# Optimization experiments

Measured on AMD Instinct MI355X. Metric: run time of the kernel, lower is better.

Reference implementation:

```python
import jax, jax.numpy as jnp
import numpy as np

N_EMB = 512
EMB_DIM = 64
COMMITMENT_COST = 0.25


def setup_inputs() -> dict:
    key = jax.random.key(0)
    k1, k2 = jax.random.split(key)
    x = jax.random.normal(k1, (32, 64, 64, EMB_DIM), dtype=jnp.float32)
    init_bound = 1.0 / N_EMB
    embedding = jax.random.uniform(k2, (N_EMB, EMB_DIM), dtype=jnp.float32,
                                   minval=-init_bound, maxval=init_bound)
    return {"x": x, "embedding": embedding}


def reference(x, embedding):
    M, D = embedding.shape
    x_flat = jax.lax.stop_gradient(x).reshape(-1, D)  # [N, D]
    # distances = (-cdist(x, E))**2 == squared euclidean distance; argmin identical
    # to argmin over cdist, computed without forming sqrt:
    d2 = (jnp.sum(x_flat * x_flat, axis=-1, keepdims=True)
          - 2.0 * (x_flat @ embedding.T)
          + jnp.sum(embedding * embedding, axis=-1))  # [N, M]
    indices = jnp.argmin(d2, axis=-1)  # [N]
    quantized = embedding[indices].reshape(x.shape)  # gather, view_as(x)

    # eval-mode (not training): commitment loss + straight-through estimator
    e_latent_loss = jnp.mean((x - jax.lax.stop_gradient(quantized)) ** 2)
    loss = COMMITMENT_COST * e_latent_loss
    quantized_st = x + jax.lax.stop_gradient(quantized - x)

    # perplexity from codebook usage (avg one-hot probabilities)
    counts = jnp.zeros((M,), dtype=jnp.float32).at[indices].add(1.0)
    avg_probs = counts / x_flat.shape[0]
    perplexity = jnp.exp(-jnp.sum(avg_probs * jnp.log(avg_probs + 1e-10)))
    return quantized_st, loss, perplexity
```

## Files before the change

### kernel.cpp

```cpp
#include <hip/hip_runtime.h>


#define D      64
#define M      512
#define N_ELEM 8388608

typedef __attribute__((ext_vector_type(8))) short short8;
typedef __attribute__((ext_vector_type(4))) float f32x4;


static __device__ __forceinline__ unsigned short f2bf(float f) {
    unsigned u = __float_as_uint(f);
    return (unsigned short)((u + 0x7FFFu + ((u >> 16) & 1u)) >> 16);
}

__global__ __launch_bounds__(512, 4)
void vq_main(const float* __restrict__ x, const float* __restrict__ emb,
             float* __restrict__ out, float* __restrict__ loss_sum,
             unsigned* __restrict__ ticket, unsigned* __restrict__ ghist) {
    __shared__ __align__(16) char sBuf[69632];
    __shared__ unsigned sHist[M];
    __shared__ unsigned sCode[256];
    __shared__ float sRed[8];
    __shared__ unsigned sLast;
    short* sE = (short*)sBuf;
    float* sX = (float*)sBuf;

    const int tid = threadIdx.x;
    const int w = tid >> 6, lane = tid & 63;
    const int q = lane >> 4, col = lane & 15;
    const int rowBase = blockIdx.x * 256 + w * 32;

    float4 xc[8];
    {
        const float* p0 = x + (size_t)(rowBase + col) * D + q * 8;
        const float* p1 = x + (size_t)(rowBase + 16 + col) * D + q * 8;
        xc[0] = *(const float4*)(p0);      xc[1] = *(const float4*)(p0 + 4);
        xc[2] = *(const float4*)(p0 + 32); xc[3] = *(const float4*)(p0 + 36);
        xc[4] = *(const float4*)(p1);      xc[5] = *(const float4*)(p1 + 4);
        xc[6] = *(const float4*)(p1 + 32); xc[7] = *(const float4*)(p1 + 36);
    }

    {
        const float4* ef4 = (const float4*)emb;
        const int swz = ((lane & 7) << 3) | (lane >> 3);
        const int base = tid & ~63;
#pragma unroll
        for (int i = 0; i < 8; ++i) {
            const int idx2 = i * 512 + base + swz;
            const float4 v0 = ef4[idx2 * 2];
            const float4 v1 = ef4[idx2 * 2 + 1];
            const int c = idx2 >> 3, p2 = idx2 & 7;
            const int s = p2 >> 2, qq = p2 & 3;
            const int ct = c >> 4, ccol = c & 15;
            short8 h;
            h[0] = (short)f2bf(-2.f * v0.x); h[1] = (short)f2bf(-2.f * v0.y);
            h[2] = (short)f2bf(-2.f * v0.z); h[3] = (short)f2bf(-2.f * v0.w);
            h[4] = (short)f2bf(-2.f * v1.x); h[5] = (short)f2bf(-2.f * v1.y);
            h[6] = (short)f2bf(-2.f * v1.z); h[7] = (short)f2bf(-2.f * v1.w);
            *(short8*)&sE[((ct * 2 + s) * 64 + qq * 16 + ccol) * 8] = h;
        }
        sHist[tid] = 0u;
    }

    short8 XH[2][2];
#pragma unroll
    for (int p = 0; p < 2; ++p) {
        float f[16] = {xc[p*4+0].x, xc[p*4+0].y, xc[p*4+0].z, xc[p*4+0].w,
                       xc[p*4+1].x, xc[p*4+1].y, xc[p*4+1].z, xc[p*4+1].w,
                       xc[p*4+2].x, xc[p*4+2].y, xc[p*4+2].z, xc[p*4+2].w,
                       xc[p*4+3].x, xc[p*4+3].y, xc[p*4+3].z, xc[p*4+3].w};
#pragma unroll
        for (int j = 0; j < 8; ++j) {
            XH[p][0][j] = (short)f2bf(f[j]);
            XH[p][1][j] = (short)f2bf(f[8 + j]);
        }
    }

    __syncthreads();

    unsigned best0 = 0xFFFFFFFFu, best1 = 0xFFFFFFFFu;
#pragma unroll 4
    for (int t = 0; t < 32; ++t) {
        const int fb = t * 1024 + lane * 8;
        short8 Eh0 = *(const short8*)&sE[fb];
        short8 Eh1 = *(const short8*)&sE[fb + 512];

        f32x4 a1 = {1.f, 1.f, 1.f, 1.f};
        a1 = __builtin_amdgcn_mfma_f32_16x16x32_bf16(Eh0, XH[0][0], a1, 0, 0, 0);
        a1 = __builtin_amdgcn_mfma_f32_16x16x32_bf16(Eh1, XH[0][1], a1, 0, 0, 0);
        f32x4 b1 = {1.f, 1.f, 1.f, 1.f};
        b1 = __builtin_amdgcn_mfma_f32_16x16x32_bf16(Eh0, XH[1][0], b1, 0, 0, 0);
        b1 = __builtin_amdgcn_mfma_f32_16x16x32_bf16(Eh1, XH[1][1], b1, 0, 0, 0);

        const int cb = t * 16 + q * 4;
#pragma unroll
        for (int r = 0; r < 4; ++r) {
            unsigned p0 = (__float_as_uint(a1[r]) & 0xFFFFFE00u) | (unsigned)(cb + r);
            unsigned p1 = (__float_as_uint(b1[r]) & 0xFFFFFE00u) | (unsigned)(cb + r);
            best0 = p0 < best0 ? p0 : best0;
            best1 = p1 < best1 ? p1 : best1;
        }
    }

    {
        unsigned o;
        o = __shfl_xor(best0, 16, 64); best0 = o < best0 ? o : best0;
        o = __shfl_xor(best0, 32, 64); best0 = o < best0 ? o : best0;
        o = __shfl_xor(best1, 16, 64); best1 = o < best1 ? o : best1;
        o = __shfl_xor(best1, 32, 64); best1 = o < best1 ? o : best1;
    }
    if (q == 0) {
        const unsigned c0 = best0 & 511u, c1 = best1 & 511u;
        sCode[w * 32 + col] = c0;
        sCode[w * 32 + 16 + col] = c1;
        atomicAdd(&sHist[c0], 1u);
        atomicAdd(&sHist[c1], 1u);
    }

    __syncthreads();

    {
        const unsigned h = sHist[tid];
        if (h) atomicAdd(&ghist[((unsigned)blockIdx.x & 7u) * 512u + tid], h);
    }

    {
        const int r0 = w * 32 + col, r1 = r0 + 16;
        *(float4*)&sX[r0 * 68 + q * 8]          = xc[0];
        *(float4*)&sX[r0 * 68 + q * 8 + 4]      = xc[1];
        *(float4*)&sX[r0 * 68 + 32 + q * 8]     = xc[2];
        *(float4*)&sX[r0 * 68 + 32 + q * 8 + 4] = xc[3];
        *(float4*)&sX[r1 * 68 + q * 8]          = xc[4];
        *(float4*)&sX[r1 * 68 + q * 8 + 4]      = xc[5];
        *(float4*)&sX[r1 * 68 + 32 + q * 8]     = xc[6];
        *(float4*)&sX[r1 * 68 + 32 + q * 8 + 4] = xc[7];
    }

    __syncthreads();

    float lacc = 0.f;
#pragma unroll
    for (int j = 0; j < 8; ++j) {
        const int idx = j * 512 + tid;
        const int row = idx >> 4, c16 = idx & 15;
        const unsigned code = sCode[row];
        const float4 xv = *(const float4*)&sX[row * 68 + c16 * 4];
        const float4 qv = *(const float4*)(emb + (size_t)code * D + c16 * 4);
        const float d0 = xv.x - qv.x, d1 = xv.y - qv.y,
                    d2 = xv.z - qv.z, d3 = xv.w - qv.w;
        lacc = fmaf(d0, d0, lacc); lacc = fmaf(d1, d1, lacc);
        lacc = fmaf(d2, d2, lacc); lacc = fmaf(d3, d3, lacc);
        float4 o;
        o.x = xv.x - d0; o.y = xv.y - d1; o.z = xv.z - d2; o.w = xv.w - d3;
        *(float4*)(out + ((size_t)blockIdx.x * 256 + row) * D + c16 * 4) = o;
    }
#pragma unroll
    for (int off = 32; off > 0; off >>= 1) lacc += __shfl_down(lacc, off, 64);
    if (lane == 0) sRed[w] = lacc;
    __syncthreads();

    if (tid == 0) {
        float s = ((sRed[0] + sRed[1]) + (sRed[2] + sRed[3]))
                + ((sRed[4] + sRed[5]) + (sRed[6] + sRed[7]));
        atomicAdd(loss_sum, s);
    }
    __syncthreads();

    if (tid == 0) {
        __threadfence();
        sLast = (atomicAdd(ticket, 1u) == 511u) ? 1u : 0u;
    }
    __syncthreads();

    if (sLast) {
        unsigned cnt = 0;
#pragma unroll
        for (int k = 0; k < 8; ++k) cnt += atomicAdd(&ghist[k * 512 + tid], 0u);
        const float p = (float)cnt * (1.0f / 131072.0f);
        float term = p * logf(p + 1e-10f);
#pragma unroll
        for (int off = 32; off > 0; off >>= 1) term += __shfl_down(term, off, 64);
        if (lane == 0) sRed[w] = term;
        __syncthreads();
        if (tid == 0) {
            float s = 0.f;
#pragma unroll
            for (int ww = 0; ww < 8; ++ww) s += sRed[ww];
            const float L = atomicAdd(loss_sum, 0.0f);
            out[N_ELEM]     = 0.25f * (L * (1.0f / 8388608.0f));
            out[N_ELEM + 1] = expf(-s);
        }
    }
}

extern "C" void kernel_launch(void* const* d_in, const int* in_sizes, int n_in,
                              void* d_out, int out_size, void* d_ws, size_t ws_size,
                              hipStream_t stream) {
    (void)in_sizes; (void)n_in; (void)out_size; (void)ws_size;
    const float* x   = (const float*)d_in[0];
    const float* emb = (const float*)d_in[1];
    float* out = (float*)d_out;

    float*    loss   = (float*)d_ws;
    unsigned* ticket = (unsigned*)((char*)d_ws + 32);
    unsigned* ghist  = (unsigned*)((char*)d_ws + 64);

    hipMemsetAsync(d_ws, 0, 64 + 8 * 512 * sizeof(unsigned), stream);

    vq_main<<<dim3(512), dim3(512), 0, stream>>>(x, emb, out, loss, ticket, ghist);
}
```

Measured before the change: 114.4 us.

## Split fused VQ kernel into argmin, output, and histogram-finalize kernels

Splits the single fused kernel into three launches. The first computes nearest-code indices via MFMA and writes them to a workspace. The second re-reads x and gathers codebook rows to produce the output and loss. A single-block kernel then builds the histogram and computes perplexity. This removes the memset, the cross-block ticket and the global histogram atomics, and lowers LDS use in the argmin kernel. In exchange it re-reads x from memory and adds two kernel launches.

```diff
diff --git a/kernel.cpp b/kernel.cpp
--- a/kernel.cpp
+++ b/kernel.cpp
@@ -8,28 +8,22 @@
 typedef __attribute__((ext_vector_type(8))) short short8;
 typedef __attribute__((ext_vector_type(4))) float f32x4;
 
-
 static __device__ __forceinline__ unsigned short f2bf(float f) {
     unsigned u = __float_as_uint(f);
     return (unsigned short)((u + 0x7FFFu + ((u >> 16) & 1u)) >> 16);
 }
 
 __global__ __launch_bounds__(512, 4)
-void vq_main(const float* __restrict__ x, const float* __restrict__ emb,
-             float* __restrict__ out, float* __restrict__ loss_sum,
-             unsigned* __restrict__ ticket, unsigned* __restrict__ ghist) {
-    __shared__ __align__(16) char sBuf[69632];
-    __shared__ unsigned sHist[M];
-    __shared__ unsigned sCode[256];
-    __shared__ float sRed[8];
-    __shared__ unsigned sLast;
-    short* sE = (short*)sBuf;
-    float* sX = (float*)sBuf;
+void vq_argmin(const float* __restrict__ x, const float* __restrict__ emb,
+               unsigned short* __restrict__ codes, float* __restrict__ loss_sum) {
+    __shared__ __align__(16) short sE[32768];
 
     const int tid = threadIdx.x;
     const int w = tid >> 6, lane = tid & 63;
     const int q = lane >> 4, col = lane & 15;
     const int rowBase = blockIdx.x * 256 + w * 32;
+
+    if (blockIdx.x == 0 && tid == 0) *loss_sum = 0.f;
 
     float4 xc[8];
     {
@@ -60,7 +54,6 @@
             h[6] = (short)f2bf(-2.f * v1.z); h[7] = (short)f2bf(-2.f * v1.w);
             *(short8*)&sE[((ct * 2 + s) * 64 + qq * 16 + ccol) * 8] = h;
         }
-        sHist[tid] = 0u;
     }
 
     short8 XH[2][2];
@@ -111,41 +104,26 @@
         o = __shfl_xor(best1, 32, 64); best1 = o < best1 ? o : best1;
     }
     if (q == 0) {
-        const unsigned c0 = best0 & 511u, c1 = best1 & 511u;
-        sCode[w * 32 + col] = c0;
-        sCode[w * 32 + 16 + col] = c1;
-        atomicAdd(&sHist[c0], 1u);
-        atomicAdd(&sHist[c1], 1u);
+        codes[blockIdx.x * 256 + w * 32 + col]      = (unsigned short)(best0 & 511u);
+        codes[blockIdx.x * 256 + w * 32 + 16 + col] = (unsigned short)(best1 & 511u);
     }
+}
 
-    __syncthreads();
-
-    {
-        const unsigned h = sHist[tid];
-        if (h) atomicAdd(&ghist[((unsigned)blockIdx.x & 7u) * 512u + tid], h);
-    }
-
-    {
-        const int r0 = w * 32 + col, r1 = r0 + 16;
-        *(float4*)&sX[r0 * 68 + q * 8]          = xc[0];
-        *(float4*)&sX[r0 * 68 + q * 8 + 4]      = xc[1];
-        *(float4*)&sX[r0 * 68 + 32 + q * 8]     = xc[2];
-        *(float4*)&sX[r0 * 68 + 32 + q * 8 + 4] = xc[3];
-        *(float4*)&sX[r1 * 68 + q * 8]          = xc[4];
-        *(float4*)&sX[r1 * 68 + q * 8 + 4]      = xc[5];
-        *(float4*)&sX[r1 * 68 + 32 + q * 8]     = xc[6];
-        *(float4*)&sX[r1 * 68 + 32 + q * 8 + 4] = xc[7];
-    }
-
-    __syncthreads();
+__global__ __launch_bounds__(256, 4)
+void vq_out_k(const float* __restrict__ x, const float* __restrict__ emb,
+              const unsigned short* __restrict__ codes, float* __restrict__ out,
+              float* __restrict__ loss_sum) {
+    __shared__ float sRed[4];
+    const int tid = threadIdx.x;
+    const int w = tid >> 6, lane = tid & 63;
 
     float lacc = 0.f;
 #pragma unroll
-    for (int j = 0; j < 8; ++j) {
-        const int idx = j * 512 + tid;
+    for (int j = 0; j < 4; ++j) {
+        const int idx = (j * 2048 + blockIdx.x) * 256 + tid;
         const int row = idx >> 4, c16 = idx & 15;
-        const unsigned code = sCode[row];
-        const float4 xv = *(const float4*)&sX[row * 68 + c16 * 4];
+        const unsigned code = codes[row];
+        const float4 xv = *(const float4*)(x + (size_t)idx * 4);
         const float4 qv = *(const float4*)(emb + (size_t)code * D + c16 * 4);
         const float d0 = xv.x - qv.x, d1 = xv.y - qv.y,
                     d2 = xv.z - qv.z, d3 = xv.w - qv.w;
@@ -153,44 +131,50 @@
         lacc = fmaf(d2, d2, lacc); lacc = fmaf(d3, d3, lacc);
         float4 o;
         o.x = xv.x - d0; o.y = xv.y - d1; o.z = xv.z - d2; o.w = xv.w - d3;
-        *(float4*)(out + ((size_t)blockIdx.x * 256 + row) * D + c16 * 4) = o;
+        *(float4*)(out + (size_t)idx * 4) = o;
     }
 #pragma unroll
     for (int off = 32; off > 0; off >>= 1) lacc += __shfl_down(lacc, off, 64);
     if (lane == 0) sRed[w] = lacc;
     __syncthreads();
+    if (tid == 0)
+        atomicAdd(loss_sum, (sRed[0] + sRed[1]) + (sRed[2] + sRed[3]));
+}
 
-    if (tid == 0) {
-        float s = ((sRed[0] + sRed[1]) + (sRed[2] + sRed[3]))
-                + ((sRed[4] + sRed[5]) + (sRed[6] + sRed[7]));
-        atomicAdd(loss_sum, s);
+__global__ __launch_bounds__(512)
+void vq_final(const unsigned short* __restrict__ codes,
+              const float* __restrict__ loss_sum, float* __restrict__ out) {
+    __shared__ unsigned sH[M];
+    __shared__ float sRed[8];
+    const int tid = threadIdx.x;
+    const int w = tid >> 6, lane = tid & 63;
+
+    sH[tid] = 0u;
+    __syncthreads();
+
+    const uint4* cv = (const uint4*)codes;
+#pragma unroll 4
+    for (int k = 0; k < 32; ++k) {
+        const uint4 v = cv[k * 512 + tid];
+        atomicAdd(&sH[v.x & 0xFFFFu], 1u); atomicAdd(&sH[v.x >> 16], 1u);
+        atomicAdd(&sH[v.y & 0xFFFFu], 1u); atomicAdd(&sH[v.y >> 16], 1u);
+        atomicAdd(&sH[v.z & 0xFFFFu], 1u); atomicAdd(&sH[v.z >> 16], 1u);
+        atomicAdd(&sH[v.w & 0xFFFFu], 1u); atomicAdd(&sH[v.w >> 16], 1u);
     }
     __syncthreads();
 
+    const float p = (float)sH[tid] * (1.0f / 131072.0f);
+    float term = p * logf(p + 1e-10f);
+#pragma unroll
+    for (int off = 32; off > 0; off >>= 1) term += __shfl_down(term, off, 64);
+    if (lane == 0) sRed[w] = term;
+    __syncthreads();
     if (tid == 0) {
-        __threadfence();
-        sLast = (atomicAdd(ticket, 1u) == 511u) ? 1u : 0u;
-    }
-    __syncthreads();
-
-    if (sLast) {
-        unsigned cnt = 0;
+        float s = 0.f;
 #pragma unroll
-        for (int k = 0; k < 8; ++k) cnt += atomicAdd(&ghist[k * 512 + tid], 0u);
-        const float p = (float)cnt * (1.0f / 131072.0f);
-        float term = p * logf(p + 1e-10f);
-#pragma unroll
-        for (int off = 32; off > 0; off >>= 1) term += __shfl_down(term, off, 64);
-        if (lane == 0) sRed[w] = term;
-        __syncthreads();
-        if (tid == 0) {
-            float s = 0.f;
-#pragma unroll
-            for (int ww = 0; ww < 8; ++ww) s += sRed[ww];
-            const float L = atomicAdd(loss_sum, 0.0f);
-            out[N_ELEM]     = 0.25f * (L * (1.0f / 8388608.0f));
-            out[N_ELEM + 1] = expf(-s);
-        }
+        for (int ww = 0; ww < 8; ++ww) s += sRed[ww];
+        out[N_ELEM]     = 0.25f * (loss_sum[0] * (1.0f / 8388608.0f));
+        out[N_ELEM + 1] = expf(-s);
     }
 }
 
@@ -202,11 +186,10 @@
     const float* emb = (const float*)d_in[1];
     float* out = (float*)d_out;
 
-    float*    loss   = (float*)d_ws;
-    unsigned* ticket = (unsigned*)((char*)d_ws + 32);
-    unsigned* ghist  = (unsigned*)((char*)d_ws + 64);
+    float*          loss  = (float*)d_ws;
+    unsigned short* codes = (unsigned short*)((char*)d_ws + 4096);
 
-    hipMemsetAsync(d_ws, 0, 64 + 8 * 512 * sizeof(unsigned), stream);
-
-    vq_main<<<dim3(512), dim3(512), 0, stream>>>(x, emb, out, loss, ticket, ghist);
+    vq_argmin<<<dim3(512),  dim3(512), 0, stream>>>(x, emb, codes, loss);
+    vq_out_k <<<dim3(2048), dim3(256), 0, stream>>>(x, emb, codes, out, loss);
+    vq_final <<<dim3(1),    dim3(512), 0, stream>>>(codes, loss, out);
 }
```

New measurement: 136.1 us. 1.19x slower.

## Replace atomic last-block reduction with per-block partials and a finalize kernel

Applied to the files above, without the earlier changes.

Each block now writes its loss partial and a 16-bit histogram slice to workspace instead of using global atomics and a ticket counter. A second single-block kernel sums all partials and computes loss and perplexity. This removes the memset, the global atomics and the threadfence/ticket serialization, at the cost of an extra kernel launch and about 512KB of partial-histogram writes and reads.

```diff
diff --git a/kernel.cpp b/kernel.cpp
--- a/kernel.cpp
+++ b/kernel.cpp
@@ -8,7 +8,6 @@
 typedef __attribute__((ext_vector_type(8))) short short8;
 typedef __attribute__((ext_vector_type(4))) float f32x4;
 
-
 static __device__ __forceinline__ unsigned short f2bf(float f) {
     unsigned u = __float_as_uint(f);
     return (unsigned short)((u + 0x7FFFu + ((u >> 16) & 1u)) >> 16);
@@ -16,13 +15,12 @@
 
 __global__ __launch_bounds__(512, 4)
 void vq_main(const float* __restrict__ x, const float* __restrict__ emb,
-             float* __restrict__ out, float* __restrict__ loss_sum,
-             unsigned* __restrict__ ticket, unsigned* __restrict__ ghist) {
+             float* __restrict__ out, float* __restrict__ lossPart,
+             unsigned short* __restrict__ partial) {
     __shared__ __align__(16) char sBuf[69632];
     __shared__ unsigned sHist[M];
     __shared__ unsigned sCode[256];
     __shared__ float sRed[8];
-    __shared__ unsigned sLast;
     short* sE = (short*)sBuf;
     float* sX = (float*)sBuf;
 
@@ -121,11 +119,6 @@
     __syncthreads();
 
     {
-        const unsigned h = sHist[tid];
-        if (h) atomicAdd(&ghist[((unsigned)blockIdx.x & 7u) * 512u + tid], h);
-    }
-
-    {
         const int r0 = w * 32 + col, r1 = r0 + 16;
         *(float4*)&sX[r0 * 68 + q * 8]          = xc[0];
         *(float4*)&sX[r0 * 68 + q * 8 + 4]      = xc[1];
@@ -160,37 +153,58 @@
     if (lane == 0) sRed[w] = lacc;
     __syncthreads();
 
+    partial[(size_t)blockIdx.x * M + tid] = (unsigned short)sHist[tid];
     if (tid == 0) {
         float s = ((sRed[0] + sRed[1]) + (sRed[2] + sRed[3]))
                 + ((sRed[4] + sRed[5]) + (sRed[6] + sRed[7]));
-        atomicAdd(loss_sum, s);
-    }
-    __syncthreads();
-
-    if (tid == 0) {
-        __threadfence();
-        sLast = (atomicAdd(ticket, 1u) == 511u) ? 1u : 0u;
-    }
-    __syncthreads();
-
-    if (sLast) {
-        unsigned cnt = 0;
-#pragma unroll
-        for (int k = 0; k < 8; ++k) cnt += atomicAdd(&ghist[k * 512 + tid], 0u);
-        const float p = (float)cnt * (1.0f / 131072.0f);
-        float term = p * logf(p + 1e-10f);
-#pragma unroll
-        for (int off = 32; off > 0; off >>= 1) term += __shfl_down(term, off, 64);
-        if (lane == 0) sRed[w] = term;
-        __syncthreads();
-        if (tid == 0) {
-            float s = 0.f;
-#pragma unroll
-            for (int ww = 0; ww < 8; ++ww) s += sRed[ww];
-            const float L = atomicAdd(loss_sum, 0.0f);
-            out[N_ELEM]     = 0.25f * (L * (1.0f / 8388608.0f));
-            out[N_ELEM + 1] = expf(-s);
-        }
+        lossPart[blockIdx.x] = s;
+    }
+}
+
+__global__ __launch_bounds__(512)
+void vq_final(const unsigned short* __restrict__ partial,
+              const float* __restrict__ lossPart, float* __restrict__ out) {
+    __shared__ unsigned sP[8][512];
+    __shared__ float sRed[8];
+    __shared__ float sLoss[8];
+    const int t = threadIdx.x;
+    const int w = t >> 6, lane = t & 63;
+    const int o = t & 63;
+    const int c = t >> 6;
+
+    float lp = lossPart[t];
+#pragma unroll
+    for (int off = 32; off > 0; off >>= 1) lp += __shfl_down(lp, off, 64);
+    if (lane == 0) sLoss[w] = lp;
+
+    unsigned acc[8] = {0, 0, 0, 0, 0, 0, 0, 0};
+#pragma unroll 8
+    for (int b = c * 64; b < c * 64 + 64; ++b) {
+        const uint4 v = *(const uint4*)(partial + (size_t)b * M + o * 8);
+        acc[0] += v.x & 0xFFFFu; acc[1] += v.x >> 16;
+        acc[2] += v.y & 0xFFFFu; acc[3] += v.y >> 16;
+        acc[4] += v.z & 0xFFFFu; acc[5] += v.z >> 16;
+        acc[6] += v.w & 0xFFFFu; acc[7] += v.w >> 16;
+    }
+#pragma unroll
+    for (int j = 0; j < 8; ++j) sP[c][o * 8 + j] = acc[j];
+    __syncthreads();
+
+    unsigned cnt = 0;
+#pragma unroll
+    for (int cc = 0; cc < 8; ++cc) cnt += sP[cc][t];
+    const float p = (float)cnt * (1.0f / 131072.0f);
+    float term = p * logf(p + 1e-10f);
+#pragma unroll
+    for (int off = 32; off > 0; off >>= 1) term += __shfl_down(term, off, 64);
+    if ((t & 63) == 0) sRed[t >> 6] = term;
+    __syncthreads();
+    if (t == 0) {
+        float s = 0.f, L = 0.f;
+#pragma unroll
+        for (int ww = 0; ww < 8; ++ww) { s += sRed[ww]; L += sLoss[ww]; }
+        out[N_ELEM]     = 0.25f * (L * (1.0f / 8388608.0f));
+        out[N_ELEM + 1] = expf(-s);
     }
 }
 
@@ -202,11 +216,9 @@
     const float* emb = (const float*)d_in[1];
     float* out = (float*)d_out;
 
-    float*    loss   = (float*)d_ws;
-    unsigned* ticket = (unsigned*)((char*)d_ws + 32);
-    unsigned* ghist  = (unsigned*)((char*)d_ws + 64);
-
-    hipMemsetAsync(d_ws, 0, 64 + 8 * 512 * sizeof(unsigned), stream);
-
-    vq_main<<<dim3(512), dim3(512), 0, stream>>>(x, emb, out, loss, ticket, ghist);
-}
+    float*          lossPart = (float*)d_ws;
+    unsigned short* part     = (unsigned short*)((char*)d_ws + 4096);
+
+    vq_main <<<dim3(512), dim3(512), 0, stream>>>(x, emb, out, lossPart, part);
+    vq_final<<<dim3(1),   dim3(512), 0, stream>>>(part, lossPart, out);
+}
```

Result: faster. 104.9 us (-8.3%).
